# Kernel optimization log

Hardware: AMD Instinct MI355X
Metric: run time of the kernel (lower is better)

Reference implementation:

```python
import jax, jax.numpy as jnp
import numpy as np

B, S, E, H, LD, P, NC = 4, 256, 256, 8, 128, 256, 2
N = S * P  # total points (static)
EPS = 1e-5


def setup_inputs() -> dict:
    key = jax.random.key(0)
    ks = jax.random.split(key, 12)
    r = lambda i, shape, s: jax.random.normal(ks[i], shape, jnp.float32) * s
    return dict(
        gl_feats=jax.random.normal(ks[0], (S, B, E), jnp.float32),
        lo_feats=jax.random.normal(ks[1], (B, N, LD), jnp.float32),
        centroids=jax.random.normal(ks[2], (B, S, 2), jnp.float32),
        np_cluster=jnp.full((S,), P, jnp.int32),
        fc1_w=r(3, (16, 2), 0.5), fc1_b=jnp.zeros(16, jnp.float32),
        fc2_w=r(4, (E, 16), 0.1), fc2_b=jnp.zeros(E, jnp.float32),
        in_proj_w=r(5, (3 * E, E), 0.05), in_proj_b=jnp.zeros(3 * E, jnp.float32),
        out_proj_w=r(6, (E, E), 0.05), out_proj_b=jnp.zeros(E, jnp.float32),
        conv2_w=r(7, (E // 2, LD + E), 0.05), conv2_b=jnp.zeros(E // 2, jnp.float32),
        bn2_gamma=jnp.ones(E // 2, jnp.float32), bn2_beta=jnp.zeros(E // 2, jnp.float32),
        bn2_mean=jnp.zeros(E // 2, jnp.float32), bn2_var=jnp.ones(E // 2, jnp.float32),
        conv3_w=r(8, (64, E // 2), 0.05), conv3_b=jnp.zeros(64, jnp.float32),
        bn3_gamma=jnp.ones(64, jnp.float32), bn3_beta=jnp.zeros(64, jnp.float32),
        bn3_mean=jnp.zeros(64, jnp.float32), bn3_var=jnp.ones(64, jnp.float32),
        conv4_w=r(9, (NC, 64), 0.05), conv4_b=jnp.zeros(NC, jnp.float32),
    )


def _bn(z, g, b, m, v):
    # inference-mode BatchNorm1d over the channel (last) axis
    return (z - m) * jax.lax.rsqrt(v + EPS) * g + b


def reference(gl_feats, lo_feats, centroids, np_cluster,
              fc1_w, fc1_b, fc2_w, fc2_b,
              in_proj_w, in_proj_b, out_proj_w, out_proj_b,
              conv2_w, conv2_b, bn2_gamma, bn2_beta, bn2_mean, bn2_var,
              conv3_w, conv3_b, bn3_gamma, bn3_beta, bn3_mean, bn3_var,
              conv4_w, conv4_b):
    # positional encoding of centroids: Linear(2,16) -> leaky_relu -> Linear(16,E)
    h = centroids @ fc1_w.T + fc1_b                      # [B,S,16]
    h = jnp.where(h >= 0, h, 0.01 * h)                   # leaky_relu_, slope 0.01
    pos = h @ fc2_w.T + fc2_b                            # [B,S,E]
    x = gl_feats.transpose(1, 0, 2) + pos                # [B,S,E] (torch MHA is seq-first)

    # MultiheadAttention (self-attn, eval-mode dropout=identity)
    qkv = x @ in_proj_w.T + in_proj_b                    # [B,S,3E]
    q, k, v = jnp.split(qkv, 3, axis=-1)
    dh = E // H
    qh = q.reshape(B, S, H, dh)
    kh = k.reshape(B, S, H, dh)
    vh = v.reshape(B, S, H, dh)
    scores = jnp.einsum('bqhd,bkhd->bhqk', qh, kh) * (1.0 / np.sqrt(dh))
    attn = jax.nn.softmax(scores, axis=-1)               # [B,H,S,S]
    ctx = jnp.einsum('bhqk,bkhd->bqhd', attn, vh).reshape(B, S, E)
    attn_out = ctx @ out_proj_w.T + out_proj_b           # [B,S,E]

    # segment-broadcast: replace the python repeat/cat loop with a gather
    cluster_ids = jnp.repeat(jnp.arange(S), np_cluster, total_repeat_length=N)  # [N]
    global_feat = attn_out[:, cluster_ids, :]            # [B,N,E]

    pc = jnp.concatenate([lo_feats, global_feat], axis=2)  # [B,N,LD+E]
    # 1x1 Conv1d == pointwise Linear over channels
    h2 = jax.nn.relu(_bn(pc @ conv2_w.T + conv2_b, bn2_gamma, bn2_beta, bn2_mean, bn2_var))
    h3 = jax.nn.relu(_bn(h2 @ conv3_w.T + conv3_b, bn3_gamma, bn3_beta, bn3_mean, bn3_var))
    out = h3 @ conv4_w.T + conv4_b                       # [B,N,NC]
    return out.transpose(0, 2, 1)                        # [B,NC,N] to match torch layout
```

## Files before the change

kernel.cpp:

```cpp
#include <hip/hip_runtime.h>

#define B_   4
#define S_   256
#define E_   256
#define H_   8
#define LD_  128
#define N_   65536
#define NC_  2

typedef __attribute__((ext_vector_type(8))) short s8v;
typedef __attribute__((ext_vector_type(4))) float f32x4;

__device__ __forceinline__ short f2bf(float f) {
  union { float f; unsigned u; } v; v.f = f;
  unsigned r = (v.u + 0x7FFFu + ((v.u >> 16) & 1u)) >> 16;
  return (short)r;
}
__device__ __forceinline__ float bf2f(short s) {
  union { float f; unsigned u; } v; v.u = ((unsigned)(unsigned short)s) << 16;
  return v.f;
}
__device__ __forceinline__ s8v pack8(float4 a, float4 b) {
  union { s8v s; unsigned u[4]; } r;
  asm("v_cvt_pk_bf16_f32 %0, %1, %2" : "=v"(r.u[0]) : "v"(a.x), "v"(a.y));
  asm("v_cvt_pk_bf16_f32 %0, %1, %2" : "=v"(r.u[1]) : "v"(a.z), "v"(a.w));
  asm("v_cvt_pk_bf16_f32 %0, %1, %2" : "=v"(r.u[2]) : "v"(b.x), "v"(b.y));
  asm("v_cvt_pk_bf16_f32 %0, %1, %2" : "=v"(r.u[3]) : "v"(b.z), "v"(b.w));
  return r.s;
}

__global__ __launch_bounds__(256) void prep_k(
    const int* __restrict__ npc, int* __restrict__ ids,
    const float* __restrict__ ipw, const float* __restrict__ opw,
    const float* __restrict__ w2, const float* __restrict__ w3,
    const float* __restrict__ b2, const float* __restrict__ g2,
    const float* __restrict__ be2, const float* __restrict__ mu2,
    const float* __restrict__ va2,
    const float* __restrict__ b3, const float* __restrict__ g3,
    const float* __restrict__ be3, const float* __restrict__ mu3,
    const float* __restrict__ va3,
    short* __restrict__ iph, short* __restrict__ ipl,
    short* __restrict__ oph, short* __restrict__ opl,
    short* __restrict__ w2bf, short* __restrict__ w3bf,
    float* __restrict__ sc2, float* __restrict__ sh2,
    float* __restrict__ sc3, float* __restrict__ sh3,
    const float* __restrict__ gl, const float* __restrict__ cen,
    const float* __restrict__ fc1w, const float* __restrict__ fc1b,
    const float* __restrict__ fc2w, const float* __restrict__ fc2b,
    short* __restrict__ Xhi, short* __restrict__ Xlo) {
  __shared__ int red[256];
  __shared__ float hsh[16];
  int bid = blockIdx.x, t = threadIdx.x;
  if (bid < 768) {
    int i = bid * 256 + t;
    if (i < 196608) {
      float v = ipw[i]; short h = f2bf(v);
      iph[i] = h; ipl[i] = f2bf(v - bf2f(h));
    }
    if (i < 65536) {
      float v = opw[i]; short h = f2bf(v);
      oph[i] = h; opl[i] = f2bf(v - bf2f(h));
    }
    if (i < 49152) w2bf[i] = f2bf(w2[i]);
    if (i < 8192)  w3bf[i] = f2bf(w3[i]);
    if (i < 128) {
      float sc = g2[i] * rsqrtf(va2[i] + 1e-5f);
      sc2[i] = sc; sh2[i] = (b2[i] - mu2[i]) * sc + be2[i];
    }
    if (i < 64) {
      float sc = g3[i] * rsqrtf(va3[i] + 1e-5f);
      sc3[i] = sc; sh3[i] = (b3[i] - mu3[i]) * sc + be3[i];
    }
  } else if (bid <= 1024) {
    int s = bid - 768;
    int val = (s == 256) ? npc[t] : ((t < s) ? npc[t] : 0);
    red[t] = val;
    __syncthreads();
    for (int off = 128; off > 0; off >>= 1) {
      if (t < off) red[t] += red[t + off];
      __syncthreads();
    }
    int st = red[0];
    if (s < 256) {
      int en = st + npc[s]; if (en > N_) en = N_;
      for (int n = st + t; n < en; n += 256) ids[n] = s;
    } else {
      for (int n = st + t; n < N_; n += 256) ids[n] = 255;
    }
  } else {
    int bs = bid - 1025;
    int b = bs >> 8, s = bs & 255;
    if (t < 16) {
      float c0 = cen[bs * 2 + 0], c1 = cen[bs * 2 + 1];
      float v = c0 * fc1w[2 * t] + c1 * fc1w[2 * t + 1] + fc1b[t];
      hsh[t] = (v >= 0.f) ? v : 0.01f * v;
    }
    __syncthreads();
    float p = fc2b[t];
#pragma unroll
    for (int j = 0; j < 16; j++) p += hsh[j] * fc2w[t * 16 + j];
    float v = gl[((size_t)s * B_ + b) * E_ + t] + p;
    short h = f2bf(v);
    Xhi[(size_t)bs * E_ + t] = h;
    Xlo[(size_t)bs * E_ + t] = f2bf(v - bf2f(h));
  }
}

__global__ __launch_bounds__(256) void gemm_x3_k(
    const short* __restrict__ Ah, const short* __restrict__ Al,
    const short* __restrict__ Wh, const short* __restrict__ Wl,
    const float* __restrict__ bias, float* __restrict__ Cf,
    int M, int N, int K) {
  __shared__ __align__(16) short gs[18432];
  const int AH = 0, AL = 4608, WH = 9216, WL = 13824;
  int t = threadIdx.x;
  int row0 = blockIdx.x * 64, col0 = blockIdx.y * 64;
  int w = t >> 6, l = t & 63, quad = l >> 4, lr = l & 15;
  int m0 = w * 16;
  int ar = t >> 2, aq = (t & 3) * 16;
  f32x4 acc[4];
#pragma unroll
  for (int i = 0; i < 4; i++) acc[i] = (f32x4)(0.f);

  for (int kc = 0; kc < K; kc += 64) {
    __syncthreads();
    {
      size_t ra = (size_t)(row0 + ar) * K + kc + aq;
      size_t rw = (size_t)(col0 + ar) * K + kc + aq;
      *(s8v*)&gs[AH + ar * 72 + aq]     = *(const s8v*)&Ah[ra];
      *(s8v*)&gs[AH + ar * 72 + aq + 8] = *(const s8v*)&Ah[ra + 8];
      *(s8v*)&gs[AL + ar * 72 + aq]     = *(const s8v*)&Al[ra];
      *(s8v*)&gs[AL + ar * 72 + aq + 8] = *(const s8v*)&Al[ra + 8];
      *(s8v*)&gs[WH + ar * 72 + aq]     = *(const s8v*)&Wh[rw];
      *(s8v*)&gs[WH + ar * 72 + aq + 8] = *(const s8v*)&Wh[rw + 8];
      *(s8v*)&gs[WL + ar * 72 + aq]     = *(const s8v*)&Wl[rw];
      *(s8v*)&gs[WL + ar * 72 + aq + 8] = *(const s8v*)&Wl[rw + 8];
    }
    __syncthreads();
#pragma unroll
    for (int ks = 0; ks < 2; ks++) {
      int ko = ks * 32 + quad * 8;
      s8v ah = *(const s8v*)&gs[AH + (m0 + lr) * 72 + ko];
      s8v al = *(const s8v*)&gs[AL + (m0 + lr) * 72 + ko];
#pragma unroll
      for (int ct = 0; ct < 4; ct++) {
        s8v bh = *(const s8v*)&gs[WH + (ct * 16 + lr) * 72 + ko];
        s8v bl = *(const s8v*)&gs[WL + (ct * 16 + lr) * 72 + ko];
        acc[ct] = __builtin_amdgcn_mfma_f32_16x16x32_bf16(ah, bh, acc[ct], 0, 0, 0);
        acc[ct] = __builtin_amdgcn_mfma_f32_16x16x32_bf16(al, bh, acc[ct], 0, 0, 0);
        acc[ct] = __builtin_amdgcn_mfma_f32_16x16x32_bf16(ah, bl, acc[ct], 0, 0, 0);
      }
    }
  }
#pragma unroll
  for (int ct = 0; ct < 4; ct++) {
    int c = col0 + ct * 16 + lr;
    float bb = bias[c];
#pragma unroll
    for (int rg = 0; rg < 4; rg++) {
      int r = row0 + m0 + quad * 4 + rg;
      Cf[(size_t)r * N + c] = acc[ct][rg] + bb;
    }
  }
}

__global__ __launch_bounds__(256) void opgemm_k(
    const short* __restrict__ Ah, const short* __restrict__ Al,
    const short* __restrict__ Wh, const short* __restrict__ Wl,
    const float* __restrict__ bias, short* __restrict__ Cb,
    int M, int N, int K) {
  __shared__ __align__(16) short gs[18432];
  const int AH = 0, AL = 4608, WH = 9216, WL = 13824;
  int t = threadIdx.x;
  int row0 = blockIdx.x * 64, col0 = blockIdx.y * 64;
  int w = t >> 6, l = t & 63, quad = l >> 4, lr = l & 15;
  int m0 = w * 16;
  int ar = t >> 2, aq = (t & 3) * 16;
  f32x4 acc[4];
#pragma unroll
  for (int i = 0; i < 4; i++) acc[i] = (f32x4)(0.f);

  for (int kc = 0; kc < K; kc += 64) {
    __syncthreads();
    {
      size_t ra = (size_t)(row0 + ar) * K + kc + aq;
      size_t rw = (size_t)(col0 + ar) * K + kc + aq;
      *(s8v*)&gs[AH + ar * 72 + aq]     = *(const s8v*)&Ah[ra];
      *(s8v*)&gs[AH + ar * 72 + aq + 8] = *(const s8v*)&Ah[ra + 8];
      *(s8v*)&gs[AL + ar * 72 + aq]     = *(const s8v*)&Al[ra];
      *(s8v*)&gs[AL + ar * 72 + aq + 8] = *(const s8v*)&Al[ra + 8];
      *(s8v*)&gs[WH + ar * 72 + aq]     = *(const s8v*)&Wh[rw];
      *(s8v*)&gs[WH + ar * 72 + aq + 8] = *(const s8v*)&Wh[rw + 8];
      *(s8v*)&gs[WL + ar * 72 + aq]     = *(const s8v*)&Wl[rw];
      *(s8v*)&gs[WL + ar * 72 + aq + 8] = *(const s8v*)&Wl[rw + 8];
    }
    __syncthreads();
#pragma unroll
    for (int ks = 0; ks < 2; ks++) {
      int ko = ks * 32 + quad * 8;
      s8v ah = *(const s8v*)&gs[AH + (m0 + lr) * 72 + ko];
      s8v al = *(const s8v*)&gs[AL + (m0 + lr) * 72 + ko];
#pragma unroll
      for (int ct = 0; ct < 4; ct++) {
        s8v bh = *(const s8v*)&gs[WH + (ct * 16 + lr) * 72 + ko];
        s8v bl = *(const s8v*)&gs[WL + (ct * 16 + lr) * 72 + ko];
        acc[ct] = __builtin_amdgcn_mfma_f32_16x16x32_bf16(ah, bh, acc[ct], 0, 0, 0);
        acc[ct] = __builtin_amdgcn_mfma_f32_16x16x32_bf16(al, bh, acc[ct], 0, 0, 0);
        acc[ct] = __builtin_amdgcn_mfma_f32_16x16x32_bf16(ah, bl, acc[ct], 0, 0, 0);
      }
    }
  }
#pragma unroll
  for (int ct = 0; ct < 4; ct++) {
    int c = col0 + ct * 16 + lr;
    float bb = bias[c];
#pragma unroll
    for (int rg = 0; rg < 4; rg++) {
      int r = row0 + m0 + quad * 4 + rg;
      Cb[(size_t)r * N + c] = f2bf(acc[ct][rg] + bb);
    }
  }
}

__global__ __launch_bounds__(256) void gbf_k(
    const short* __restrict__ A, const short* __restrict__ w2bf,
    float* __restrict__ C) {
  __shared__ __align__(16) short gs[9216];
  const int AH = 0, BH = 4608;
  int t = threadIdx.x;
  int row0 = blockIdx.x * 64, col0 = blockIdx.y * 64;
  int w = t >> 6, l = t & 63, quad = l >> 4, lr = l & 15;
  int m0 = w * 16;
  int ar = t >> 2, aq = (t & 3) * 16;
  f32x4 acc[4];
#pragma unroll
  for (int i = 0; i < 4; i++) acc[i] = (f32x4)(0.f);

  for (int kc = 0; kc < 256; kc += 64) {
    __syncthreads();
    {
      size_t ra = (size_t)(row0 + ar) * 256 + kc + aq;
      size_t rb = (size_t)(col0 + ar) * 384 + 128 + kc + aq;
      *(s8v*)&gs[AH + ar * 72 + aq]     = *(const s8v*)&A[ra];
      *(s8v*)&gs[AH + ar * 72 + aq + 8] = *(const s8v*)&A[ra + 8];
      *(s8v*)&gs[BH + ar * 72 + aq]     = *(const s8v*)&w2bf[rb];
      *(s8v*)&gs[BH + ar * 72 + aq + 8] = *(const s8v*)&w2bf[rb + 8];
    }
    __syncthreads();
#pragma unroll
    for (int ks = 0; ks < 2; ks++) {
      int ko = ks * 32 + quad * 8;
      s8v a = *(const s8v*)&gs[AH + (m0 + lr) * 72 + ko];
#pragma unroll
      for (int ct = 0; ct < 4; ct++) {
        s8v b = *(const s8v*)&gs[BH + (ct * 16 + lr) * 72 + ko];
        acc[ct] = __builtin_amdgcn_mfma_f32_16x16x32_bf16(a, b, acc[ct], 0, 0, 0);
      }
    }
  }
#pragma unroll
  for (int ct = 0; ct < 4; ct++) {
    int c = col0 + ct * 16 + lr;
#pragma unroll
    for (int rg = 0; rg < 4; rg++) {
      int r = row0 + m0 + quad * 4 + rg;
      C[(size_t)r * 128 + c] = acc[ct][rg];
    }
  }
}

__global__ __launch_bounds__(256) void attn_k(const float* __restrict__ qkv,
                                              short* __restrict__ Chi,
                                              short* __restrict__ Clo) {
  int bid = blockIdx.x;
  int qt = bid & 7, h = (bid >> 3) & 7, b = bid >> 6;
  __shared__ __align__(16) float smem[16384];
  float* Kx = smem;
  float* Vx = smem + 8192;
  int t = threadIdx.x;
#pragma unroll
  for (int i = 0; i < 8; i++) {
    int row = i * 32 + (t >> 3);
    int d4 = (t & 7) * 4;
    const float* base = qkv + (size_t)(b * S_ + row) * 768 + h * 32 + d4;
    *(float4*)&Kx[row * 32 + d4] = *(const float4*)(base + 256);
    *(float4*)&Vx[row * 32 + d4] = *(const float4*)(base + 512);
  }
  int r = t & 31, g = t >> 5;
  float q[32];
  {
    const float* qb = qkv + (size_t)(b * S_ + qt * 32 + r) * 768 + h * 32;
#pragma unroll
    for (int d4 = 0; d4 < 32; d4 += 4) {
      float4 v = *(const float4*)(qb + d4);
      q[d4] = v.x; q[d4 + 1] = v.y; q[d4 + 2] = v.z; q[d4 + 3] = v.w;
    }
  }
  __syncthreads();
  const float scale = 0.17677669529663687f;
  int kk0 = g * 32;
  float sc[32];
  float m = -1e30f;
#pragma unroll
  for (int kk = 0; kk < 32; kk++) {
    const float* kr = &Kx[(kk0 + kk) * 32];
    float4 a = (float4){0.f, 0.f, 0.f, 0.f};
#pragma unroll
    for (int d4 = 0; d4 < 32; d4 += 4) {
      float4 kv = *(const float4*)(kr + d4);
      a.x += q[d4] * kv.x; a.y += q[d4 + 1] * kv.y;
      a.z += q[d4 + 2] * kv.z; a.w += q[d4 + 3] * kv.w;
    }
    float s = ((a.x + a.y) + (a.z + a.w)) * scale;
    sc[kk] = s;
    m = fmaxf(m, s);
  }
  float lsum = 0.f;
  float ctx[32];
#pragma unroll
  for (int d = 0; d < 32; d++) ctx[d] = 0.f;
#pragma unroll
  for (int kk = 0; kk < 32; kk++) {
    const float* vr = &Vx[(kk0 + kk) * 32];
    float p = __expf(sc[kk] - m);
    lsum += p;
#pragma unroll
    for (int d4 = 0; d4 < 32; d4 += 4) {
      float4 vv = *(const float4*)(vr + d4);
      ctx[d4] += p * vv.x; ctx[d4 + 1] += p * vv.y;
      ctx[d4 + 2] += p * vv.z; ctx[d4 + 3] += p * vv.w;
    }
  }
  __syncthreads();
  float* ctxbuf = smem;
  float* mbuf = smem + 8192;
  float* lbuf = smem + 8448;
  mbuf[g * 32 + r] = m;
  lbuf[g * 32 + r] = lsum;
#pragma unroll
  for (int d = 0; d < 32; d++)
    ctxbuf[(g * 32 + r) * 32 + ((d + r) & 31)] = ctx[d];
  __syncthreads();
  int r2 = t & 31, dq = t >> 5;
  float M = -1e30f;
#pragma unroll
  for (int gg = 0; gg < 8; gg++) M = fmaxf(M, mbuf[gg * 32 + r2]);
  float wg[8]; float L = 0.f;
#pragma unroll
  for (int gg = 0; gg < 8; gg++) {
    wg[gg] = __expf(mbuf[gg * 32 + r2] - M);
    L += lbuf[gg * 32 + r2] * wg[gg];
  }
  float invL = 1.f / L;
  size_t base = (size_t)(b * S_ + qt * 32 + r2) * E_ + h * 32;
#pragma unroll
  for (int dd = 0; dd < 4; dd++) {
    int d = dq * 4 + dd;
    float o = 0.f;
#pragma unroll
    for (int gg = 0; gg < 8; gg++)
      o += ctxbuf[(gg * 32 + r2) * 32 + ((d + r2) & 31)] * wg[gg];
    o *= invL;
    short hi = f2bf(o);
    Chi[base + d] = hi;
    Clo[base + d] = f2bf(o - bf2f(hi));
  }
}

__global__ __launch_bounds__(256, 4) void conv_fused_k(
    const float* __restrict__ lo, const float* __restrict__ G,
    const int* __restrict__ ids,
    const short* __restrict__ w2bf, const short* __restrict__ w3bf,
    const float* __restrict__ sc2, const float* __restrict__ sh2,
    const float* __restrict__ sc3, const float* __restrict__ sh3,
    const float* __restrict__ w4, const float* __restrict__ b4,
    float* __restrict__ out) {
  __shared__ __align__(16) short smem[17408];
  __shared__ int lds_ids[128];
  int t = threadIdx.x;
  int bid = blockIdx.x;
  int b = bid >> 9;
  int n0 = (bid & 511) << 7;
  int w = t >> 6, l = t & 63;
  int quad = l >> 4, lr = l & 15;
  int mh = w & 1, chh = w >> 1;
  int ar = t >> 1, akh = (t & 1) * 64;
  const float* lob = &lo[((size_t)b * N_ + n0 + ar) * LD_ + akh];

  if (t < 128) lds_ids[t] = ids[n0 + t];
  {
    float4 pf[8];
#pragma unroll
    for (int j = 0; j < 8; j++) pf[j] = *(const float4*)(lob + j * 4);
#pragma unroll
    for (int j = 0; j < 4; j++)
      *(s8v*)&smem[ar * 136 + akh + j * 8] = pack8(pf[2 * j], pf[2 * j + 1]);
#pragma unroll
    for (int j = 0; j < 8; j++) pf[j] = *(const float4*)(lob + 32 + j * 4);
#pragma unroll
    for (int j = 0; j < 4; j++)
      *(s8v*)&smem[ar * 136 + akh + 32 + j * 8] = pack8(pf[2 * j], pf[2 * j + 1]);
  }
  __syncthreads();

  f32x4 acc2[4][4];
#pragma unroll
  for (int mt = 0; mt < 4; mt++)
#pragma unroll
    for (int rg = 0; rg < 4; rg++) {
      int p = 64 * mh + 16 * mt + 4 * quad + rg;
      const float* gr = &G[((size_t)b * 256 + lds_ids[p]) * 128 + 64 * chh + lr];
#pragma unroll
      for (int ct = 0; ct < 4; ct++)
        acc2[mt][ct][rg] = gr[16 * ct];
    }

#pragma unroll
  for (int ks = 0; ks < 4; ks++) {
    int ko = ks * 32 + quad * 8;
    s8v af[4], bfr[4];
#pragma unroll
    for (int mt = 0; mt < 4; mt++)
      af[mt] = *(const s8v*)&smem[(64 * mh + 16 * mt + lr) * 136 + ko];
#pragma unroll
    for (int ct = 0; ct < 4; ct++)
      bfr[ct] = *(const s8v*)&w2bf[(size_t)(64 * chh + 16 * ct + lr) * 384 + ko];
#pragma unroll
    for (int mt = 0; mt < 4; mt++)
#pragma unroll
      for (int ct = 0; ct < 4; ct++)
        acc2[mt][ct] = __builtin_amdgcn_mfma_f32_16x16x32_bf16(af[mt], bfr[ct], acc2[mt][ct], 0, 0, 0);
  }
  __syncthreads();

#pragma unroll
  for (int ct = 0; ct < 4; ct++) {
    int c = 64 * chh + 16 * ct + lr;
    float sc = sc2[c], sh = sh2[c];
#pragma unroll
    for (int mt = 0; mt < 4; mt++)
#pragma unroll
      for (int rg = 0; rg < 4; rg++) {
        int p = 64 * mh + 16 * mt + 4 * quad + rg;
        float z = acc2[mt][ct][rg] * sc + sh;
        smem[p * 136 + c] = f2bf(fmaxf(z, 0.f));
      }
  }
  __syncthreads();

  f32x4 acc3[2][4];
#pragma unroll
  for (int i = 0; i < 2; i++)
#pragma unroll
    for (int j = 0; j < 4; j++) acc3[i][j] = (f32x4)(0.f);
#pragma unroll
  for (int ks = 0; ks < 4; ks++) {
    int ko = ks * 32 + quad * 8;
    s8v af2[2], bf3[4];
#pragma unroll
    for (int mt = 0; mt < 2; mt++)
      af2[mt] = *(const s8v*)&smem[(32 * w + 16 * mt + lr) * 136 + ko];
#pragma unroll
    for (int ct = 0; ct < 4; ct++)
      bf3[ct] = *(const s8v*)&w3bf[(size_t)(16 * ct + lr) * 128 + ko];
#pragma unroll
    for (int mt = 0; mt < 2; mt++)
#pragma unroll
      for (int ct = 0; ct < 4; ct++)
        acc3[mt][ct] = __builtin_amdgcn_mfma_f32_16x16x32_bf16(af2[mt], bf3[ct], acc3[mt][ct], 0, 0, 0);
  }
  __syncthreads();

#pragma unroll
  for (int ct = 0; ct < 4; ct++) {
    int c = 16 * ct + lr;
    float sc = sc3[c], sh = sh3[c];
#pragma unroll
    for (int mt = 0; mt < 2; mt++)
#pragma unroll
      for (int rg = 0; rg < 4; rg++) {
        int p = 32 * w + 16 * mt + 4 * quad + rg;
        float z = acc3[mt][ct][rg] * sc + sh;
        smem[p * 72 + c] = f2bf(fmaxf(z, 0.f));
      }
  }
  __syncthreads();

  {
    int c = t >> 7, p = t & 127;
    float s = b4[c];
#pragma unroll
    for (int j = 0; j < 8; j++) {
      s8v hv = *(const s8v*)&smem[p * 72 + j * 8];
#pragma unroll
      for (int e = 0; e < 8; e++)
        s += bf2f(hv[e]) * w4[c * 64 + j * 8 + e];
    }
    out[((size_t)b * NC_ + c) * N_ + n0 + p] = s;
  }
}

extern "C" void kernel_launch(void* const* d_in, const int* in_sizes, int n_in,
                              void* d_out, int out_size, void* d_ws, size_t ws_size,
                              hipStream_t stream) {
  const float* gl   = (const float*)d_in[0];
  const float* lo   = (const float*)d_in[1];
  const float* cen  = (const float*)d_in[2];
  const int*   npc  = (const int*)d_in[3];
  const float* fc1w = (const float*)d_in[4];
  const float* fc1b = (const float*)d_in[5];
  const float* fc2w = (const float*)d_in[6];
  const float* fc2b = (const float*)d_in[7];
  const float* ipw  = (const float*)d_in[8];
  const float* ipb  = (const float*)d_in[9];
  const float* opw  = (const float*)d_in[10];
  const float* opb  = (const float*)d_in[11];
  const float* w2   = (const float*)d_in[12];
  const float* b2   = (const float*)d_in[13];
  const float* g2   = (const float*)d_in[14];
  const float* be2  = (const float*)d_in[15];
  const float* mu2  = (const float*)d_in[16];
  const float* va2  = (const float*)d_in[17];
  const float* w3   = (const float*)d_in[18];
  const float* b3   = (const float*)d_in[19];
  const float* g3   = (const float*)d_in[20];
  const float* be3  = (const float*)d_in[21];
  const float* mu3  = (const float*)d_in[22];
  const float* va3  = (const float*)d_in[23];
  const float* w4   = (const float*)d_in[24];
  const float* b4   = (const float*)d_in[25];

  char* ws = (char*)d_ws;
  float* qkv  = (float*)(ws);
  short* AO   = (short*)(ws);
  short* Xhi  = (short*)(ws + 3145728);
  short* Xlo  = (short*)(ws + 3670016);
  short* Chi  = (short*)(ws + 4194304);
  short* Clo  = (short*)(ws + 4718592);
  float* G    = (float*)(ws + 5242880);
  short* iph  = (short*)(ws + 5767168);
  short* ipl  = (short*)(ws + 6160384);
  short* oph  = (short*)(ws + 6553600);
  short* opl  = (short*)(ws + 6684672);
  short* w2bf = (short*)(ws + 6815744);
  short* w3bf = (short*)(ws + 6914048);
  int*   ids  = (int*)  (ws + 6930432);
  float* sc2  = (float*)(ws + 7192576);
  float* sh2  = (float*)(ws + 7193088);
  float* sc3  = (float*)(ws + 7193600);
  float* sh3  = (float*)(ws + 7193856);
  float* out  = (float*)d_out;

  prep_k<<<2049, 256, 0, stream>>>(npc, ids, ipw, opw, w2, w3,
                                   b2, g2, be2, mu2, va2,
                                   b3, g3, be3, mu3, va3,
                                   iph, ipl, oph, opl, w2bf, w3bf,
                                   sc2, sh2, sc3, sh3,
                                   gl, cen, fc1w, fc1b, fc2w, fc2b, Xhi, Xlo);
  gemm_x3_k<<<dim3(16, 12), 256, 0, stream>>>(Xhi, Xlo, iph, ipl, ipb,
                                              qkv, B_ * S_, 768, E_);
  attn_k<<<B_ * H_ * 8, 256, 0, stream>>>(qkv, Chi, Clo);
  opgemm_k<<<dim3(16, 4), 256, 0, stream>>>(Chi, Clo, oph, opl, opb, AO,
                                            B_ * S_, 256, E_);
  gbf_k<<<dim3(16, 2), 256, 0, stream>>>(AO, w2bf, G);
  conv_fused_k<<<B_ * (N_ / 128), 256, 0, stream>>>(
      lo, G, ids, w2bf, w3bf, sc2, sh2, sc3, sh3, w4, b4, out);
}
```

Measured before the change: 301.2 us.

## Halve conv tile to 64 points, add uniform-cluster G fast path

Shrinks the fused conv kernel tile from 128 to 64 points per block, doubling the grid and raising the occupancy hint to 6 blocks per CU. The per-point gathered global features are no longer loaded as accumulator seeds. When the whole tile falls in one cluster, a single G row per channel is folded into the BN shift; otherwise G is gathered in the epilogue. The conv3 stage is re-split across waves by output channel, and the software bf16 rounding is replaced by the hardware cvt instruction. Smaller tiles mean more per-block overhead and weight reloads from global memory, while the tighter launch bound risks register spills.

```diff
diff --git a/kernel.cpp b/kernel.cpp
--- a/kernel.cpp
+++ b/kernel.cpp
@@ -12,9 +12,9 @@
 typedef __attribute__((ext_vector_type(4))) float f32x4;
 
 __device__ __forceinline__ short f2bf(float f) {
-  union { float f; unsigned u; } v; v.f = f;
-  unsigned r = (v.u + 0x7FFFu + ((v.u >> 16) & 1u)) >> 16;
-  return (short)r;
+  unsigned u;
+  asm("v_cvt_pk_bf16_f32 %0, %1, %2" : "=v"(u) : "v"(f), "v"(f));
+  return (short)u;
 }
 __device__ __forceinline__ float bf2f(short s) {
   union { float f; unsigned u; } v; v.u = ((unsigned)(unsigned short)s) << 16;
@@ -367,7 +367,7 @@
   }
 }
 
-__global__ __launch_bounds__(256, 4) void conv_fused_k(
+__global__ __launch_bounds__(256, 6) void conv_fused_k(
     const float* __restrict__ lo, const float* __restrict__ G,
     const int* __restrict__ ids,
     const short* __restrict__ w2bf, const short* __restrict__ w3bf,
@@ -375,119 +375,124 @@
     const float* __restrict__ sc3, const float* __restrict__ sh3,
     const float* __restrict__ w4, const float* __restrict__ b4,
     float* __restrict__ out) {
-  __shared__ __align__(16) short smem[17408];
-  __shared__ int lds_ids[128];
+  __shared__ __align__(16) short smem[8704];
+  __shared__ int lds_ids[64];
   int t = threadIdx.x;
   int bid = blockIdx.x;
-  int b = bid >> 9;
-  int n0 = (bid & 511) << 7;
+  int b = bid >> 10;
+  int n0 = (bid & 1023) << 6;
   int w = t >> 6, l = t & 63;
   int quad = l >> 4, lr = l & 15;
-  int mh = w & 1, chh = w >> 1;
-  int ar = t >> 1, akh = (t & 1) * 64;
-  const float* lob = &lo[((size_t)b * N_ + n0 + ar) * LD_ + akh];
-
-  if (t < 128) lds_ids[t] = ids[n0 + t];
+  int rh = w & 1, chh = w >> 1;
+
+  int id0 = ids[n0], id63 = ids[n0 + 63];
+  bool uni = (id0 == id63);
+  float gseed[4];
   {
+    const float* gr = &G[((size_t)b * 256 + id0) * 128 + 64 * chh + lr];
+#pragma unroll
+    for (int ct = 0; ct < 4; ct++) gseed[ct] = gr[16 * ct];
+  }
+  if (!uni && t < 64) lds_ids[t] = ids[n0 + t];
+
+  {
+    int ar = t >> 2, ak = (t & 3) * 32;
+    const float* lob = &lo[((size_t)b * N_ + n0 + ar) * LD_ + ak];
     float4 pf[8];
 #pragma unroll
     for (int j = 0; j < 8; j++) pf[j] = *(const float4*)(lob + j * 4);
 #pragma unroll
     for (int j = 0; j < 4; j++)
-      *(s8v*)&smem[ar * 136 + akh + j * 8] = pack8(pf[2 * j], pf[2 * j + 1]);
-#pragma unroll
-    for (int j = 0; j < 8; j++) pf[j] = *(const float4*)(lob + 32 + j * 4);
-#pragma unroll
-    for (int j = 0; j < 4; j++)
-      *(s8v*)&smem[ar * 136 + akh + 32 + j * 8] = pack8(pf[2 * j], pf[2 * j + 1]);
-  }
-  __syncthreads();
-
-  f32x4 acc2[4][4];
-#pragma unroll
-  for (int mt = 0; mt < 4; mt++)
-#pragma unroll
-    for (int rg = 0; rg < 4; rg++) {
-      int p = 64 * mh + 16 * mt + 4 * quad + rg;
-      const float* gr = &G[((size_t)b * 256 + lds_ids[p]) * 128 + 64 * chh + lr];
-#pragma unroll
-      for (int ct = 0; ct < 4; ct++)
-        acc2[mt][ct][rg] = gr[16 * ct];
-    }
-
+      *(s8v*)&smem[ar * 136 + ak + j * 8] = pack8(pf[2 * j], pf[2 * j + 1]);
+  }
+  __syncthreads();
+
+  f32x4 acc2[2][4];
+#pragma unroll
+  for (int i = 0; i < 2; i++)
+#pragma unroll
+    for (int j = 0; j < 4; j++) acc2[i][j] = (f32x4)(0.f);
 #pragma unroll
   for (int ks = 0; ks < 4; ks++) {
     int ko = ks * 32 + quad * 8;
-    s8v af[4], bfr[4];
-#pragma unroll
-    for (int mt = 0; mt < 4; mt++)
-      af[mt] = *(const s8v*)&smem[(64 * mh + 16 * mt + lr) * 136 + ko];
+    s8v af[2], bfr[4];
+#pragma unroll
+    for (int mt = 0; mt < 2; mt++)
+      af[mt] = *(const s8v*)&smem[(32 * rh + 16 * mt + lr) * 136 + ko];
 #pragma unroll
     for (int ct = 0; ct < 4; ct++)
       bfr[ct] = *(const s8v*)&w2bf[(size_t)(64 * chh + 16 * ct + lr) * 384 + ko];
 #pragma unroll
-    for (int mt = 0; mt < 4; mt++)
+    for (int mt = 0; mt < 2; mt++)
 #pragma unroll
       for (int ct = 0; ct < 4; ct++)
         acc2[mt][ct] = __builtin_amdgcn_mfma_f32_16x16x32_bf16(af[mt], bfr[ct], acc2[mt][ct], 0, 0, 0);
   }
   __syncthreads();
 
+  size_t gbase = (size_t)b * 256 * 128;
 #pragma unroll
   for (int ct = 0; ct < 4; ct++) {
     int c = 64 * chh + 16 * ct + lr;
     float sc = sc2[c], sh = sh2[c];
-#pragma unroll
-    for (int mt = 0; mt < 4; mt++)
+    float gsh = fmaf(gseed[ct], sc, sh);
+#pragma unroll
+    for (int mt = 0; mt < 2; mt++)
 #pragma unroll
       for (int rg = 0; rg < 4; rg++) {
-        int p = 64 * mh + 16 * mt + 4 * quad + rg;
-        float z = acc2[mt][ct][rg] * sc + sh;
+        int p = 32 * rh + 16 * mt + 4 * quad + rg;
+        float z;
+        if (uni) {
+          z = fmaf(acc2[mt][ct][rg], sc, gsh);
+        } else {
+          float gv = G[gbase + (size_t)lds_ids[p] * 128 + c];
+          z = fmaf(acc2[mt][ct][rg] + gv, sc, sh);
+        }
         smem[p * 136 + c] = f2bf(fmaxf(z, 0.f));
       }
   }
   __syncthreads();
 
-  f32x4 acc3[2][4];
+  f32x4 acc3[2][2];
 #pragma unroll
   for (int i = 0; i < 2; i++)
 #pragma unroll
-    for (int j = 0; j < 4; j++) acc3[i][j] = (f32x4)(0.f);
+    for (int j = 0; j < 2; j++) acc3[i][j] = (f32x4)(0.f);
 #pragma unroll
   for (int ks = 0; ks < 4; ks++) {
     int ko = ks * 32 + quad * 8;
-    s8v af2[2], bf3[4];
+    s8v af2[2], bf3[2];
 #pragma unroll
     for (int mt = 0; mt < 2; mt++)
-      af2[mt] = *(const s8v*)&smem[(32 * w + 16 * mt + lr) * 136 + ko];
-#pragma unroll
-    for (int ct = 0; ct < 4; ct++)
-      bf3[ct] = *(const s8v*)&w3bf[(size_t)(16 * ct + lr) * 128 + ko];
+      af2[mt] = *(const s8v*)&smem[(32 * rh + 16 * mt + lr) * 136 + ko];
+#pragma unroll
+    for (int ct = 0; ct < 2; ct++)
+      bf3[ct] = *(const s8v*)&w3bf[(size_t)(32 * chh + 16 * ct + lr) * 128 + ko];
 #pragma unroll
     for (int mt = 0; mt < 2; mt++)
 #pragma unroll
-      for (int ct = 0; ct < 4; ct++)
+      for (int ct = 0; ct < 2; ct++)
         acc3[mt][ct] = __builtin_amdgcn_mfma_f32_16x16x32_bf16(af2[mt], bf3[ct], acc3[mt][ct], 0, 0, 0);
   }
   __syncthreads();
 
 #pragma unroll
-  for (int ct = 0; ct < 4; ct++) {
-    int c = 16 * ct + lr;
+  for (int ct = 0; ct < 2; ct++) {
+    int c = 32 * chh + 16 * ct + lr;
     float sc = sc3[c], sh = sh3[c];
 #pragma unroll
     for (int mt = 0; mt < 2; mt++)
 #pragma unroll
       for (int rg = 0; rg < 4; rg++) {
-        int p = 32 * w + 16 * mt + 4 * quad + rg;
+        int p = 32 * rh + 16 * mt + 4 * quad + rg;
         float z = acc3[mt][ct][rg] * sc + sh;
         smem[p * 72 + c] = f2bf(fmaxf(z, 0.f));
       }
   }
   __syncthreads();
 
-  {
-    int c = t >> 7, p = t & 127;
+  if (t < 128) {
+    int c = t >> 6, p = t & 63;
     float s = b4[c];
 #pragma unroll
     for (int j = 0; j < 8; j++) {
@@ -563,6 +568,6 @@
   opgemm_k<<<dim3(16, 4), 256, 0, stream>>>(Chi, Clo, oph, opl, opb, AO,
                                             B_ * S_, 256, E_);
   gbf_k<<<dim3(16, 2), 256, 0, stream>>>(AO, w2bf, G);
-  conv_fused_k<<<B_ * (N_ / 128), 256, 0, stream>>>(
+  conv_fused_k<<<B_ * (N_ / 64), 256, 0, stream>>>(
       lo, G, ids, w2bf, w3bf, sc2, sh2, sc3, sh3, w4, b4, out);
 }
```

Result: slower. 324.3 us (+7.7%).
